# Optimization experiments

Measured on AMD Instinct MI355X. Metric: run time of the kernel, lower is better.

## Reference

```python
import jax, jax.numpy as jnp
import numpy as np

D_MODEL = 256
D_FFN = 1024
N_HEADS = 8
N_LEVELS = 4
N_POINTS = 4
SPATIAL = np.array([[60, 100], [30, 50], [15, 25], [8, 13]], dtype=np.int32)  # (H, W) per level


def _layer_norm(x, g, b, eps=1e-5):
    mu = jnp.mean(x, axis=-1, keepdims=True)
    var = jnp.mean(jnp.square(x - mu), axis=-1, keepdims=True)
    return (x - mu) * jax.lax.rsqrt(var + eps) * g + b


def _bilinear_sample(v_l, loc, aw, H, W):
    # v_l: (B,H,W,h,hd); loc: (B,Lq,h,p,2) normalized [0,1]; aw: (B,Lq,h,p)
    B = v_l.shape[0]
    h = v_l.shape[3]
    x = loc[..., 0] * W - 0.5  # grid_sample align_corners=False convention
    y = loc[..., 1] * H - 0.5
    x0 = jnp.floor(x)
    y0 = jnp.floor(y)
    lx = x - x0
    ly = y - y0
    x0i = x0.astype(jnp.int32)
    y0i = y0.astype(jnp.int32)
    bi = jnp.arange(B)[:, None, None, None]
    hi = jnp.arange(h)[None, None, :, None]

    def g(xi, yi):
        valid = (xi >= 0) & (xi < W) & (yi >= 0) & (yi < H)
        xc = jnp.clip(xi, 0, W - 1)
        yc = jnp.clip(yi, 0, H - 1)
        return v_l[bi, yc, xc, hi] * valid[..., None].astype(v_l.dtype)  # zero padding

    w00 = (1 - lx) * (1 - ly)
    w01 = lx * (1 - ly)
    w10 = (1 - lx) * ly
    w11 = lx * ly
    samp = (g(x0i, y0i) * w00[..., None] + g(x0i + 1, y0i) * w01[..., None]
            + g(x0i, y0i + 1) * w10[..., None] + g(x0i + 1, y0i + 1) * w11[..., None])
    # weighted sum over sampling points -> (B,Lq,h,hd)
    return jnp.einsum('blhpd,blhp->blhd', samp, aw)


def _msda(q, val, ref, W_value, b_value, W_off, b_off, W_attn, b_attn, W_out, b_out):
    # mmcv MultiScaleDeformableAttention (batch_first, identity=query, eval-mode dropout)
    B, Lq, C = q.shape
    hd = C // N_HEADS
    v = (val @ W_value + b_value).reshape(B, -1, N_HEADS, hd)
    off = (q @ W_off + b_off).reshape(B, Lq, N_HEADS, N_LEVELS, N_POINTS, 2)
    aw = jax.nn.softmax((q @ W_attn + b_attn).reshape(B, Lq, N_HEADS, N_LEVELS * N_POINTS), axis=-1)
    aw = aw.reshape(B, Lq, N_HEADS, N_LEVELS, N_POINTS)
    normalizer = jnp.asarray(SPATIAL[:, ::-1].copy(), dtype=q.dtype)  # (levels, 2) = (W, H)
    loc = ref[:, :, None, :, None, :] + off / normalizer[None, None, None, :, None, :]
    out = jnp.zeros((B, Lq, N_HEADS, hd), q.dtype)
    start = 0
    for lvl in range(N_LEVELS):
        H, W = int(SPATIAL[lvl, 0]), int(SPATIAL[lvl, 1])
        v_l = v[:, start:start + H * W].reshape(B, H, W, N_HEADS, hd)
        start += H * W
        out = out + _bilinear_sample(v_l, loc[:, :, :, lvl], aw[:, :, :, lvl], H, W)
    return q + out.reshape(B, Lq, C) @ W_out + b_out  # identity + output_proj


def setup_inputs() -> dict:
    key = jax.random.key(0)
    ks = jax.random.split(key, 16)
    bs, cams, nq = 1, 6, 6400
    l = int(SPATIAL.prod(axis=1).sum())
    s = 0.02
    inp = {
        'query': jax.random.normal(ks[0], (bs, nq, D_MODEL), jnp.float32),
        'key': jax.random.normal(ks[1], (bs, cams, l, D_MODEL), jnp.float32),
        'value': jax.random.normal(ks[2], (bs, cams, l, D_MODEL), jnp.float32),
        'reference_points_cam': jax.random.uniform(ks[3], (cams, bs, nq, N_LEVELS, 2), jnp.float32),
        'spatial_shapes': jnp.asarray(SPATIAL),
        'level_start_index': jnp.asarray(np.concatenate([[0], np.cumsum(SPATIAL.prod(axis=1))[:-1]]).astype(np.int32)),
        'bev_mask': jax.random.randint(ks[4], (cams, bs, nq, 4), 0, 2).astype(jnp.int32),
        'W_value': jax.random.normal(ks[5], (D_MODEL, D_MODEL), jnp.float32) * s,
        'b_value': jnp.zeros((D_MODEL,), jnp.float32),
        'W_off': jax.random.normal(ks[6], (D_MODEL, N_HEADS * N_LEVELS * N_POINTS * 2), jnp.float32) * s,
        'b_off': jax.random.normal(ks[7], (N_HEADS * N_LEVELS * N_POINTS * 2,), jnp.float32) * s,
        'W_attn': jax.random.normal(ks[8], (D_MODEL, N_HEADS * N_LEVELS * N_POINTS), jnp.float32) * s,
        'b_attn': jnp.zeros((N_HEADS * N_LEVELS * N_POINTS,), jnp.float32),
        'W_out': jax.random.normal(ks[9], (D_MODEL, D_MODEL), jnp.float32) * s,
        'b_out': jnp.zeros((D_MODEL,), jnp.float32),
        'ln1_g': jnp.ones((D_MODEL,), jnp.float32),
        'ln1_b': jnp.zeros((D_MODEL,), jnp.float32),
        'W1': jax.random.normal(ks[10], (D_MODEL, D_FFN), jnp.float32) * s,
        'b1': jnp.zeros((D_FFN,), jnp.float32),
        'W2': jax.random.normal(ks[11], (D_FFN, D_MODEL), jnp.float32) * s,
        'b2': jnp.zeros((D_MODEL,), jnp.float32),
        'ln2_g': jnp.ones((D_MODEL,), jnp.float32),
        'ln2_b': jnp.zeros((D_MODEL,), jnp.float32),
    }
    return inp


def reference(query, key, value, reference_points_cam, spatial_shapes, level_start_index, bev_mask,
              W_value, b_value, W_off, b_off, W_attn, b_attn, W_out, b_out,
              ln1_g, ln1_b, W1, b1, W2, b2, ln2_g, ln2_b):
    bs, nq, C = query.shape
    cams = key.shape[1]
    l = key.shape[2]
    # per-camera query visibility taken from batch element 0 (as in original)
    cam_mask = (bev_mask[:, 0].sum(-1) > 0).astype(query.dtype)  # (cams, nq)
    # rebatch via masking: equivalent to gather-to-padded since attention is per-query
    q_rb = (query[:, None] * cam_mask[None, :, :, None]).reshape(bs * cams, nq, C)
    ref_rb = (jnp.transpose(reference_points_cam, (1, 0, 2, 3, 4))
              * cam_mask[None, :, :, None, None]).reshape(bs * cams, nq, N_LEVELS, 2)
    val = value.reshape(bs * cams, l, C)
    attn = _msda(q_rb, val, ref_rb, W_value, b_value, W_off, b_off, W_attn, b_attn, W_out, b_out)
    attn = attn.reshape(bs, cams, nq, C)
    # scatter-add back (only visible camera contributions)
    slots = jnp.einsum('bknc,kn->bnc', attn, cam_mask)
    # visibility count (full bev_mask, per batch element)
    count = (bev_mask.sum(-1) > 0).astype(query.dtype)  # (cams, bs, nq)
    count = jnp.maximum(count.transpose(1, 2, 0).sum(-1), 1.0)  # (bs, nq)
    slots = slots / count[..., None]
    x = _layer_norm(slots + query, ln1_g, ln1_b)
    ffn = jax.nn.relu(x @ W1 + b1) @ W2 + b2
    return _layer_norm(x + ffn, ln2_g, ln2_b)
```

## Files before the change

kernel.cpp:

```cpp
#include <hip/hip_runtime.h>
#include <math.h>

#define NQ      6400
#define NCAMS   6
#define LTOT    7979
#define DM      256
#define DFFN    1024

typedef __attribute__((ext_vector_type(8))) short bf16x8;
typedef __attribute__((ext_vector_type(4))) float f32x4;

__device__ inline unsigned short f32_to_bf16(float f) {
    unsigned u = __float_as_uint(f);
    unsigned r = u + 0x7FFF + ((u >> 16) & 1);
    return (unsigned short)(r >> 16);
}

__global__ __launch_bounds__(256) void wt_kernel(
    const float* __restrict__ Wv, const float* __restrict__ Woff,
    const float* __restrict__ Wattn, const float* __restrict__ Wout,
    const float* __restrict__ W1, const float* __restrict__ W2,
    unsigned short* __restrict__ wsT)
{
    int b = blockIdx.x;
    const float* src; int K, N, t0, dstoff;
    if (b < 64)       { src = Wv;    K = 256;  N = 256;  t0 = 0;   dstoff = 0; }
    else if (b < 128) { src = Woff;  K = 256;  N = 256;  t0 = 64;  dstoff = 65536; }
    else if (b < 160) { src = Wattn; K = 256;  N = 128;  t0 = 128; dstoff = 131072; }
    else if (b < 224) { src = Wout;  K = 256;  N = 256;  t0 = 160; dstoff = 163840; }
    else if (b < 480) { src = W1;    K = 256;  N = 1024; t0 = 224; dstoff = 229376; }
    else              { src = W2;    K = 1024; N = 256;  t0 = 480; dstoff = 491520; }
    int t = b - t0;
    int ntn = N >> 5;
    int kt = t / ntn, nt = t - kt * ntn;
    __shared__ float tile[32][33];
    int tx = threadIdx.x & 31, ty = threadIdx.x >> 5;
    #pragma unroll
    for (int i = 0; i < 4; ++i)
        tile[ty + i * 8][tx] = src[(size_t)(kt * 32 + ty + i * 8) * N + nt * 32 + tx];
    __syncthreads();
    #pragma unroll
    for (int i = 0; i < 4; ++i) {
        int nn = nt * 32 + ty + i * 8;
        wsT[dstoff + (size_t)nn * K + kt * 32 + tx] = f32_to_bf16(tile[tx][ty + i * 8]);
    }
}

__global__ __launch_bounds__(256) void gemm_v_kernel(
    const float* __restrict__ A, const unsigned short* __restrict__ BT,
    const float* __restrict__ bias, unsigned short* __restrict__ Cb, int M)
{
    const int K = 256;
    __shared__ __align__(16) unsigned short As[128][40];
    __shared__ __align__(16) unsigned short Bs[128][40];

    const int tid  = threadIdx.x;
    const int wave = tid >> 6, lane = tid & 63;
    const int wm = wave >> 1, wn = wave & 1;
    const int quad = lane >> 4, l16 = lane & 15;
    const int m0 = blockIdx.y * 128, n0 = blockIdx.x * 128;

    f32x4 acc[4][4] = {};

    for (int k0 = 0; k0 < K; k0 += 32) {
        #pragma unroll
        for (int i = 0; i < 2; ++i) {
            int idx = tid + 256 * i;
            int r = idx >> 2, kc = (idx & 3) * 8;
            int gr = m0 + r;
            float4 f0, f1;
            if (gr < M) {
                f0 = *(const float4*)(A + (size_t)gr * K + k0 + kc);
                f1 = *(const float4*)(A + (size_t)gr * K + k0 + kc + 4);
            } else { f0 = make_float4(0,0,0,0); f1 = f0; }
            uint4 o;
            o.x = f32_to_bf16(f0.x) | ((unsigned)f32_to_bf16(f0.y) << 16);
            o.y = f32_to_bf16(f0.z) | ((unsigned)f32_to_bf16(f0.w) << 16);
            o.z = f32_to_bf16(f1.x) | ((unsigned)f32_to_bf16(f1.y) << 16);
            o.w = f32_to_bf16(f1.z) | ((unsigned)f32_to_bf16(f1.w) << 16);
            *(uint4*)&As[r][kc] = o;
        }
        #pragma unroll
        for (int i = 0; i < 2; ++i) {
            int idx = tid + 256 * i;
            int r = idx >> 2, kc = (idx & 3) * 8;
            *(uint4*)&Bs[r][kc] = *(const uint4*)(BT + (size_t)(n0 + r) * K + k0 + kc);
        }
        __syncthreads();
        bf16x8 af[4], bfr[4];
        #pragma unroll
        for (int mi = 0; mi < 4; ++mi)
            af[mi] = *(const bf16x8*)&As[wm * 64 + mi * 16 + l16][quad * 8];
        #pragma unroll
        for (int ni = 0; ni < 4; ++ni)
            bfr[ni] = *(const bf16x8*)&Bs[wn * 64 + ni * 16 + l16][quad * 8];
        #pragma unroll
        for (int mi = 0; mi < 4; ++mi)
            #pragma unroll
            for (int ni = 0; ni < 4; ++ni)
                acc[mi][ni] = __builtin_amdgcn_mfma_f32_16x16x32_bf16(
                    af[mi], bfr[ni], acc[mi][ni], 0, 0, 0);
        __syncthreads();
    }

    #pragma unroll
    for (int mi = 0; mi < 4; ++mi) {
        #pragma unroll
        for (int r = 0; r < 4; ++r) {
            int gm = m0 + wm * 64 + mi * 16 + quad * 4 + r;
            if (gm >= M) continue;
            int cam = gm / LTOT;
            int pix = gm - cam * LTOT;
            #pragma unroll
            for (int ni = 0; ni < 4; ++ni) {
                int gn = n0 + wn * 64 + ni * 16 + l16;
                int head = gn >> 5, ch = gn & 31;
                float v = acc[mi][ni][r] + bias[gn];
                Cb[(((size_t)(cam * 8 + head)) * LTOT + pix) * 32 + ch] = f32_to_bf16(v);
            }
        }
    }
}

__global__ __launch_bounds__(256) void qproj_kernel(
    const float* __restrict__ A, const unsigned short* __restrict__ WqT,
    const float* __restrict__ b_off, const float* __restrict__ b_attn,
    float* __restrict__ qoff, float* __restrict__ qaw)
{
    const int K = 256;
    __shared__ __align__(16) unsigned short As[64][40];
    __shared__ __align__(16) unsigned short Bs[128][40];

    const int tid  = threadIdx.x;
    const int wave = tid >> 6, lane = tid & 63;
    const int wm = wave >> 1, wn = wave & 1;
    const int quad = lane >> 4, l16 = lane & 15;
    const int m0 = blockIdx.y * 64, n0 = blockIdx.x * 128;
    const int is_attn = (n0 == 256);

    f32x4 acc[2][4] = {};

    for (int k0 = 0; k0 < K; k0 += 32) {
        {
            int r = tid >> 2, kc = (tid & 3) * 8;
            float4 f0 = *(const float4*)(A + (size_t)(m0 + r) * K + k0 + kc);
            float4 f1 = *(const float4*)(A + (size_t)(m0 + r) * K + k0 + kc + 4);
            uint4 o;
            o.x = f32_to_bf16(f0.x) | ((unsigned)f32_to_bf16(f0.y) << 16);
            o.y = f32_to_bf16(f0.z) | ((unsigned)f32_to_bf16(f0.w) << 16);
            o.z = f32_to_bf16(f1.x) | ((unsigned)f32_to_bf16(f1.y) << 16);
            o.w = f32_to_bf16(f1.z) | ((unsigned)f32_to_bf16(f1.w) << 16);
            *(uint4*)&As[r][kc] = o;
        }
        #pragma unroll
        for (int i = 0; i < 2; ++i) {
            int idx = tid + 256 * i;
            int r = idx >> 2, kc = (idx & 3) * 8;
            *(uint4*)&Bs[r][kc] = *(const uint4*)(WqT + (size_t)(n0 + r) * K + k0 + kc);
        }
        __syncthreads();
        bf16x8 af[2], bfr[4];
        #pragma unroll
        for (int mi = 0; mi < 2; ++mi)
            af[mi] = *(const bf16x8*)&As[wm * 32 + mi * 16 + l16][quad * 8];
        #pragma unroll
        for (int ni = 0; ni < 4; ++ni)
            bfr[ni] = *(const bf16x8*)&Bs[wn * 64 + ni * 16 + l16][quad * 8];
        #pragma unroll
        for (int mi = 0; mi < 2; ++mi)
            #pragma unroll
            for (int ni = 0; ni < 4; ++ni)
                acc[mi][ni] = __builtin_amdgcn_mfma_f32_16x16x32_bf16(
                    af[mi], bfr[ni], acc[mi][ni], 0, 0, 0);
        __syncthreads();
    }

    if (is_attn) {
        #pragma unroll
        for (int mi = 0; mi < 2; ++mi) {
            #pragma unroll
            for (int r = 0; r < 4; ++r) {
                int gm = m0 + wm * 32 + mi * 16 + quad * 4 + r;
                #pragma unroll
                for (int ni = 0; ni < 4; ++ni) {
                    int gn = wn * 64 + ni * 16 + l16;
                    float v = acc[mi][ni][r] + b_attn[gn];
                    float mx = v;
                    #pragma unroll
                    for (int s = 1; s < 16; s <<= 1)
                        mx = fmaxf(mx, __shfl_xor(mx, s, 64));
                    float e = __expf(v - mx);
                    float sum = e;
                    #pragma unroll
                    for (int s = 1; s < 16; s <<= 1)
                        sum += __shfl_xor(sum, s, 64);
                    qaw[(size_t)gm * 128 + gn] = e / sum;
                }
            }
        }
    } else {
        #pragma unroll
        for (int mi = 0; mi < 2; ++mi) {
            #pragma unroll
            for (int r = 0; r < 4; ++r) {
                int gm = m0 + wm * 32 + mi * 16 + quad * 4 + r;
                #pragma unroll
                for (int ni = 0; ni < 4; ++ni) {
                    int gn = n0 + wn * 64 + ni * 16 + l16;
                    qoff[(size_t)gm * 256 + gn] = acc[mi][ni][r] + b_off[gn];
                }
            }
        }
    }
}

__global__ __launch_bounds__(256) void sample_kernel(
    const unsigned short* __restrict__ vb,
    const float* __restrict__ qoff,
    const float* __restrict__ aw,
    const float* __restrict__ refpts,
    const int*   __restrict__ bev_mask,
    unsigned short* __restrict__ outsum,
    float* __restrict__ visb)
{
    const int bid = blockIdx.x;
    const int h   = bid & 7;
    const int q0  = (bid >> 3) * 16;
    const int tid = threadIdx.x;
    const int sq  = tid >> 4;
    const int tup = tid & 15;
    const int lvl = tup >> 2;
    const int n_s = q0 + sq;
    const int tg  = (tid >> 2) & 3;
    const int cg  = tid & 3;

    __shared__ int2  s_tab[2][4][272];
    __shared__ float s_vis[NCAMS][16];
    __shared__ int   s_cnt[NCAMS];
    __shared__ int   s_nvis[16];

    if (tid < 96) {
        int cam = tid >> 4, q = tid & 15;
        const int* bm = bev_mask + ((size_t)cam * NQ + q0 + q) * 4;
        s_vis[cam][q] = ((bm[0] + bm[1] + bm[2] + bm[3]) > 0) ? 1.f : 0.f;
    }
    __syncthreads();
    if (tid < NCAMS) {
        float s = 0.f;
        #pragma unroll
        for (int q = 0; q < 16; ++q) s += s_vis[tid][q];
        s_cnt[tid] = (int)s;
    }
    if (tid >= 32 && tid < 48) {
        int q = tid - 32;
        float s = 0.f;
        #pragma unroll
        for (int cam = 0; cam < NCAMS; ++cam) s += s_vis[cam][q];
        s_nvis[q] = (int)s;
    }
    __syncthreads();

    const float my_aw = aw[(size_t)n_s * 128 + h * 16 + tup];
    const float offx  = qoff[(size_t)n_s * 256 + h * 32 + tup * 2];
    const float offy  = qoff[(size_t)n_s * 256 + h * 32 + tup * 2 + 1];
    const int Wl   = (lvl == 0) ? 100 : (lvl == 1) ? 50 : (lvl == 2) ? 25 : 13;
    const int Hl   = (lvl == 0) ? 60  : (lvl == 1) ? 30 : (lvl == 2) ? 15 : 8;
    const int base = (lvl == 0) ? 0   : (lvl == 1) ? 6000 : (lvl == 2) ? 7500 : 7875;
    const float dx = offx / (float)Wl;
    const float dy = offy / (float)Hl;
    const int tabi = sq * 17 + tup;

    int vcams[NCAMS], nvc = 0;
    #pragma unroll
    for (int k = 0; k < NCAMS; ++k)
        if (s_cnt[k] > 0) vcams[nvc++] = k;

    auto build_tab = [&](int k, int buf) {
        const size_t rbase = (((size_t)k * NQ + n_s) * 4 + lvl) * 2;
        float fx = (refpts[rbase + 0] + dx) * (float)Wl - 0.5f;
        float fy = (refpts[rbase + 1] + dy) * (float)Hl - 0.5f;
        float x0f = floorf(fx), y0f = floorf(fy);
        float lx = fx - x0f, ly = fy - y0f;
        int x0 = (int)x0f, y0 = (int)y0f;
        int x1 = x0 + 1, y1 = y0 + 1;
        float wb = my_aw * s_vis[k][sq];
        float w00 = (1.f - lx) * (1.f - ly) * wb;
        float w01 = lx * (1.f - ly) * wb;
        float w10 = (1.f - lx) * ly * wb;
        float w11 = lx * ly * wb;
        bool vx0 = (x0 >= 0) & (x0 < Wl), vx1 = (x1 >= 0) & (x1 < Wl);
        bool vy0 = (y0 >= 0) & (y0 < Hl), vy1 = (y1 >= 0) & (y1 < Hl);
        s_tab[buf][0][tabi] = make_int2((vx0 & vy0) ? (base + y0 * Wl + x0) * 64 : 0,
                                        __float_as_int((vx0 & vy0) ? w00 : 0.f));
        s_tab[buf][1][tabi] = make_int2((vx1 & vy0) ? (base + y0 * Wl + x1) * 64 : 0,
                                        __float_as_int((vx1 & vy0) ? w01 : 0.f));
        s_tab[buf][2][tabi] = make_int2((vx0 & vy1) ? (base + y1 * Wl + x0) * 64 : 0,
                                        __float_as_int((vx0 & vy1) ? w10 : 0.f));
        s_tab[buf][3][tabi] = make_int2((vx1 & vy1) ? (base + y1 * Wl + x1) * 64 : 0,
                                        __float_as_int((vx1 & vy1) ? w11 : 0.f));
    };

    float a0 = 0.f, a1 = 0.f, a2 = 0.f, a3 = 0.f;
    float a4 = 0.f, a5 = 0.f, a6 = 0.f, a7 = 0.f;

    if (nvc > 0) build_tab(vcams[0], 0);
    __syncthreads();

    int pb = 0;
    for (int i = 0; i < nvc; ++i) {
        int k = vcams[i];
        if (i + 1 < nvc) build_tab(vcams[i + 1], pb ^ 1);
        const char* vkh = (const char*)vb + (size_t)(k * 8 + h) * (LTOT * 64) + cg * 16;
        #pragma unroll
        for (int j = 0; j < 4; ++j) {
            int ti = sq * 17 + tg * 4 + j;
            #pragma unroll
            for (int corner = 0; corner < 4; ++corner) {
                int2 t = s_tab[pb][corner][ti];
                float w = __int_as_float(t.y);
                uint4 d = *(const uint4*)(vkh + t.x);
                a0 += w * __uint_as_float(d.x << 16);
                a1 += w * __uint_as_float(d.x & 0xFFFF0000u);
                a2 += w * __uint_as_float(d.y << 16);
                a3 += w * __uint_as_float(d.y & 0xFFFF0000u);
                a4 += w * __uint_as_float(d.z << 16);
                a5 += w * __uint_as_float(d.z & 0xFFFF0000u);
                a6 += w * __uint_as_float(d.w << 16);
                a7 += w * __uint_as_float(d.w & 0xFFFF0000u);
            }
        }
        __syncthreads();
        pb ^= 1;
    }

    a0 += __shfl_xor(a0, 4, 64); a0 += __shfl_xor(a0, 8, 64);
    a1 += __shfl_xor(a1, 4, 64); a1 += __shfl_xor(a1, 8, 64);
    a2 += __shfl_xor(a2, 4, 64); a2 += __shfl_xor(a2, 8, 64);
    a3 += __shfl_xor(a3, 4, 64); a3 += __shfl_xor(a3, 8, 64);
    a4 += __shfl_xor(a4, 4, 64); a4 += __shfl_xor(a4, 8, 64);
    a5 += __shfl_xor(a5, 4, 64); a5 += __shfl_xor(a5, 8, 64);
    a6 += __shfl_xor(a6, 4, 64); a6 += __shfl_xor(a6, 8, 64);
    a7 += __shfl_xor(a7, 4, 64); a7 += __shfl_xor(a7, 8, 64);

    if ((tid & 12) == 0) {
        int nv = s_nvis[sq];
        float sc = 1.f / (float)(nv > 0 ? nv : 1);
        uint4 o;
        o.x = f32_to_bf16(a0 * sc) | ((unsigned)f32_to_bf16(a1 * sc) << 16);
        o.y = f32_to_bf16(a2 * sc) | ((unsigned)f32_to_bf16(a3 * sc) << 16);
        o.z = f32_to_bf16(a4 * sc) | ((unsigned)f32_to_bf16(a5 * sc) << 16);
        o.w = f32_to_bf16(a6 * sc) | ((unsigned)f32_to_bf16(a7 * sc) << 16);
        *(uint4*)(outsum + (size_t)n_s * 256 + h * 32 + cg * 8) = o;
    }
    if (h == 0 && tid < 16) visb[q0 + tid] = (s_nvis[tid] > 0) ? 1.f : 0.f;
}

__global__ __launch_bounds__(256) void projln1_kernel(
    const unsigned short* __restrict__ A, const unsigned short* __restrict__ BT,
    const float* __restrict__ query, const float* __restrict__ visb,
    const float* __restrict__ b_out, const float* __restrict__ g,
    const float* __restrict__ b,
    float* __restrict__ xout, unsigned short* __restrict__ xbf)
{
    const int K = 256;
    __shared__ __align__(16) unsigned short As[32][40];
    __shared__ __align__(16) unsigned short Bs[256][40];
    __shared__ float sred[2][4][4][2];
    __shared__ float ssred[2][4][4][2];
    __shared__ float s_mu[32], s_rs[32];

    const int tid  = threadIdx.x;
    const int wave = tid >> 6, lane = tid & 63;
    const int wm = wave >> 1, wn = wave & 1;
    const int quad = lane >> 4, l16 = lane & 15;
    const int m0 = blockIdx.x * 32;

    f32x4 acc[8] = {};

    for (int k0 = 0; k0 < K; k0 += 32) {
        {
            int r = tid >> 3, kc = (tid & 7) * 4;
            *(uint2*)&As[r][kc] = *(const uint2*)(A + (size_t)(m0 + r) * K + k0 + kc);
        }
        {
            const unsigned short* src = BT + (size_t)tid * K + k0;
            uint4 d0 = *(const uint4*)(src);
            uint4 d1 = *(const uint4*)(src + 8);
            uint4 d2 = *(const uint4*)(src + 16);
            uint4 d3 = *(const uint4*)(src + 24);
            *(uint4*)&Bs[tid][0]  = d0;
            *(uint4*)&Bs[tid][8]  = d1;
            *(uint4*)&Bs[tid][16] = d2;
            *(uint4*)&Bs[tid][24] = d3;
        }
        __syncthreads();
        bf16x8 af = *(const bf16x8*)&As[wm * 16 + l16][quad * 8];
        #pragma unroll
        for (int ni = 0; ni < 8; ++ni) {
            bf16x8 bfr = *(const bf16x8*)&Bs[wn * 128 + ni * 16 + l16][quad * 8];
            acc[ni] = __builtin_amdgcn_mfma_f32_16x16x32_bf16(af, bfr, acc[ni], 0, 0, 0);
        }
        __syncthreads();
    }

    float vals[8][4];
    #pragma unroll
    for (int r = 0; r < 4; ++r) {
        int gm = m0 + wm * 16 + quad * 4 + r;
        float vs = visb[gm];
        float s = 0.f, ss = 0.f;
        #pragma unroll
        for (int ni = 0; ni < 8; ++ni) {
            int gn = wn * 128 + ni * 16 + l16;
            float v = acc[ni][r] + vs * b_out[gn]
                    + query[(size_t)gm * 256 + gn] * (1.f + vs);
            vals[ni][r] = v;
            s += v; ss += v * v;
        }
        #pragma unroll
        for (int m = 1; m < 16; m <<= 1) {
            s  += __shfl_xor(s,  m, 64);
            ss += __shfl_xor(ss, m, 64);
        }
        if (l16 == 0) {
            sred[wm][quad][r][wn]  = s;
            ssred[wm][quad][r][wn] = ss;
        }
    }
    __syncthreads();
    if (tid < 32) {
        int lwm = tid >> 4, lq = (tid >> 2) & 3, lr = tid & 3;
        float s  = sred[lwm][lq][lr][0]  + sred[lwm][lq][lr][1];
        float ss = ssred[lwm][lq][lr][0] + ssred[lwm][lq][lr][1];
        float mu = s * (1.f / 256.f);
        float var = ss * (1.f / 256.f) - mu * mu;
        s_mu[tid] = mu;
        s_rs[tid] = rsqrtf(var + 1e-5f);
    }
    __syncthreads();

    #pragma unroll
    for (int r = 0; r < 4; ++r) {
        int rowl = wm * 16 + quad * 4 + r;
        int gm = m0 + rowl;
        float mu = s_mu[rowl], rs = s_rs[rowl];
        #pragma unroll
        for (int ni = 0; ni < 8; ++ni) {
            int gn = wn * 128 + ni * 16 + l16;
            float res = (vals[ni][r] - mu) * rs * g[gn] + b[gn];
            xout[(size_t)gm * 256 + gn] = res;
            xbf[(size_t)gm * 256 + gn] = f32_to_bf16(res);
        }
    }
}

__global__ __launch_bounds__(256) void gemm64_kernel(
    const unsigned short* __restrict__ A, const unsigned short* __restrict__ BT,
    const float* __restrict__ bias, float* __restrict__ C,
    unsigned short* __restrict__ Cb,
    int M, int N, int K, int mode)
{
    __shared__ __align__(16) unsigned short As[64][40];
    __shared__ __align__(16) unsigned short Bs[128][40];

    const int tid  = threadIdx.x;
    const int wave = tid >> 6, lane = tid & 63;
    const int wm = wave >> 1, wn = wave & 1;
    const int quad = lane >> 4, l16 = lane & 15;
    const int m0 = blockIdx.y * 64, n0 = blockIdx.x * 128;
    const int nz = gridDim.z;
    const int klen = K / nz;
    const int kbase = blockIdx.z * klen;

    f32x4 acc[2][4] = {};

    for (int k0 = kbase; k0 < kbase + klen; k0 += 32) {
        {
            int r = tid >> 2, kc = (tid & 3) * 8;
            int gr = m0 + r;
            uint4 d = (gr < M) ? *(const uint4*)(A + (size_t)gr * K + k0 + kc)
                               : make_uint4(0u, 0u, 0u, 0u);
            *(uint4*)&As[r][kc] = d;
        }
        #pragma unroll
        for (int i = 0; i < 2; ++i) {
            int idx = tid + 256 * i;
            int r = idx >> 2, kc = (idx & 3) * 8;
            *(uint4*)&Bs[r][kc] = *(const uint4*)(BT + (size_t)(n0 + r) * K + k0 + kc);
        }
        __syncthreads();
        bf16x8 af[2], bfr[4];
        #pragma unroll
        for (int mi = 0; mi < 2; ++mi)
            af[mi] = *(const bf16x8*)&As[wm * 32 + mi * 16 + l16][quad * 8];
        #pragma unroll
        for (int ni = 0; ni < 4; ++ni)
            bfr[ni] = *(const bf16x8*)&Bs[wn * 64 + ni * 16 + l16][quad * 8];
        #pragma unroll
        for (int mi = 0; mi < 2; ++mi)
            #pragma unroll
            for (int ni = 0; ni < 4; ++ni)
                acc[mi][ni] = __builtin_amdgcn_mfma_f32_16x16x32_bf16(
                    af[mi], bfr[ni], acc[mi][ni], 0, 0, 0);
        __syncthreads();
    }

    const float* bz = (blockIdx.z == 0) ? bias : nullptr;
    float* Cz = C ? (C + (size_t)blockIdx.z * M * N) : nullptr;

    #pragma unroll
    for (int mi = 0; mi < 2; ++mi) {
        #pragma unroll
        for (int r = 0; r < 4; ++r) {
            int gm = m0 + wm * 32 + mi * 16 + quad * 4 + r;
            if (gm >= M) continue;
            #pragma unroll
            for (int ni = 0; ni < 4; ++ni) {
                int gn = n0 + wn * 64 + ni * 16 + l16;
                float v = acc[mi][ni][r] + (bz ? bz[gn] : 0.f);
                if (mode == 1) {
                    Cb[(size_t)gm * N + gn] = f32_to_bf16(fmaxf(v, 0.f));
                } else {
                    Cz[(size_t)gm * N + gn] = v;
                }
            }
        }
    }
}

__device__ inline float block_sum_256(float v, float* red)
{
    #pragma unroll
    for (int o = 32; o > 0; o >>= 1) v += __shfl_down(v, o, 64);
    int lane = threadIdx.x & 63, w = threadIdx.x >> 6;
    if (lane == 0) red[w] = v;
    __syncthreads();
    float t = red[0] + red[1] + red[2] + red[3];
    __syncthreads();
    return t;
}

__global__ __launch_bounds__(256) void ln2_kernel(
    const float* __restrict__ x, const float* __restrict__ f0,
    const float* __restrict__ f1,
    const float* __restrict__ g, const float* __restrict__ b,
    float* __restrict__ out)
{
    __shared__ float red[4];
    int n = blockIdx.x, j = threadIdx.x;
    size_t idx = (size_t)n * 256 + j;
    float t = x[idx] + f0[idx] + f1[idx];
    float mu = block_sum_256(t, red) * (1.f / 256.f);
    float d = t - mu;
    float var = block_sum_256(d * d, red) * (1.f / 256.f);
    out[idx] = d * rsqrtf(var + 1e-5f) * g[j] + b[j];
}

extern "C" void kernel_launch(void* const* d_in, const int* in_sizes, int n_in,
                              void* d_out, int out_size, void* d_ws, size_t ws_size,
                              hipStream_t stream)
{
    const float* query   = (const float*)d_in[0];
    const float* value   = (const float*)d_in[2];
    const float* refpts  = (const float*)d_in[3];
    const int*   bevmask = (const int*)d_in[6];
    const float* W_value = (const float*)d_in[7];
    const float* b_value = (const float*)d_in[8];
    const float* W_off   = (const float*)d_in[9];
    const float* b_off   = (const float*)d_in[10];
    const float* W_attn  = (const float*)d_in[11];
    const float* b_attn  = (const float*)d_in[12];
    const float* W_out   = (const float*)d_in[13];
    const float* b_out   = (const float*)d_in[14];
    const float* ln1_g   = (const float*)d_in[15];
    const float* ln1_b   = (const float*)d_in[16];
    const float* W1      = (const float*)d_in[17];
    const float* b1      = (const float*)d_in[18];
    const float* W2      = (const float*)d_in[19];
    const float* b2      = (const float*)d_in[20];
    const float* ln2_g   = (const float*)d_in[21];
    const float* ln2_b   = (const float*)d_in[22];
    float* out = (float*)d_out;

    char* ws = (char*)d_ws;
    unsigned short* vb     = (unsigned short*)(ws + 0);
    float*          xbuf   = (float*)(ws + 0);
    unsigned short* xbf    = (unsigned short*)(ws + 7000000);
    unsigned short* hbf    = (unsigned short*)(ws + 11000000);
    float*          qoff   = (float*)(ws + 25000000);
    float*          qaw    = (float*)(ws + 32000000);
    unsigned short* outsum = (unsigned short*)(ws + 35300000);
    float*          visb   = (float*)(ws + 38600000);
    unsigned short* wsT    = (unsigned short*)(ws + 38700000);
    float*          ffnout = (float*)(ws + 41000000);

    unsigned short* WvT = wsT;
    unsigned short* WqT = wsT + 65536;
    unsigned short* WoT = wsT + 163840;
    unsigned short* W1T = wsT + 229376;
    unsigned short* W2T = wsT + 491520;

    const int MV = NCAMS * LTOT;

    wt_kernel<<<dim3(736), 256, 0, stream>>>(
        W_value, W_off, W_attn, W_out, W1, W2, wsT);
    gemm_v_kernel<<<dim3(2, (MV + 127) / 128), 256, 0, stream>>>(
        value, WvT, b_value, vb, MV);
    qproj_kernel<<<dim3(3, 100), 256, 0, stream>>>(
        query, WqT, b_off, b_attn, qoff, qaw);
    sample_kernel<<<dim3(3200), 256, 0, stream>>>(
        vb, qoff, qaw, refpts, bevmask, outsum, visb);
    projln1_kernel<<<dim3(200), 256, 0, stream>>>(
        outsum, WoT, query, visb, b_out, ln1_g, ln1_b, xbuf, xbf);
    gemm64_kernel<<<dim3(8, 100, 1), 256, 0, stream>>>(
        xbf, W1T, b1, nullptr, hbf, NQ, DFFN, 256, 1);
    gemm64_kernel<<<dim3(2, 100, 2), 256, 0, stream>>>(
        hbf, W2T, b2, ffnout, nullptr, NQ, 256, DFFN, 0);
    ln2_kernel<<<dim3(NQ), 256, 0, stream>>>(
        xbuf, ffnout, ffnout + (size_t)NQ * 256, ln2_g, ln2_b, out);
}
```

Baseline: 321.7 us.

## Fuse FFN2 with LayerNorm2, enlarge FFN1 tiles, precompute all camera sample tables

Replaces the split-K FFN2 GEMM and the separate LayerNorm kernel with one kernel. It computes a full 256-wide output row block, adds bias and residual, and applies LayerNorm in registers, which removes the fp32 partial-sum round trip and one launch. FFN1 now uses a specialised 128x128 tile kernel. The sampling kernel builds the tables for all six cameras up front instead of double-buffering, which removes per-camera barriers but enlarges shared memory use and does table work for cameras with no visible queries. The fused FFN2 grid has only 200 blocks with a long K loop, so parallelism may be low.

```diff
diff --git a/kernel.cpp b/kernel.cpp
--- a/kernel.cpp
+++ b/kernel.cpp
@@ -234,7 +234,7 @@
     const int tg  = (tid >> 2) & 3;
     const int cg  = tid & 3;
 
-    __shared__ int2  s_tab[2][4][272];
+    __shared__ int2  s_tab[NCAMS][4][272];
     __shared__ float s_vis[NCAMS][16];
     __shared__ int   s_cnt[NCAMS];
     __shared__ int   s_nvis[16];
@@ -258,7 +258,6 @@
         for (int cam = 0; cam < NCAMS; ++cam) s += s_vis[cam][q];
         s_nvis[q] = (int)s;
     }
-    __syncthreads();
 
     const float my_aw = aw[(size_t)n_s * 128 + h * 16 + tup];
     const float offx  = qoff[(size_t)n_s * 256 + h * 32 + tup * 2];
@@ -270,15 +269,16 @@
     const float dy = offy / (float)Hl;
     const int tabi = sq * 17 + tup;
 
-    int vcams[NCAMS], nvc = 0;
+    float2 rp[NCAMS];
     #pragma unroll
     for (int k = 0; k < NCAMS; ++k)
-        if (s_cnt[k] > 0) vcams[nvc++] = k;
-
-    auto build_tab = [&](int k, int buf) {
-        const size_t rbase = (((size_t)k * NQ + n_s) * 4 + lvl) * 2;
-        float fx = (refpts[rbase + 0] + dx) * (float)Wl - 0.5f;
-        float fy = (refpts[rbase + 1] + dy) * (float)Hl - 0.5f;
+        rp[k] = *(const float2*)(refpts + (((size_t)k * NQ + n_s) * 4 + lvl) * 2);
+    __syncthreads();
+
+    #pragma unroll
+    for (int k = 0; k < NCAMS; ++k) {
+        float fx = (rp[k].x + dx) * (float)Wl - 0.5f;
+        float fy = (rp[k].y + dy) * (float)Hl - 0.5f;
         float x0f = floorf(fx), y0f = floorf(fy);
         float lx = fx - x0f, ly = fy - y0f;
         int x0 = (int)x0f, y0 = (int)y0f;
@@ -290,33 +290,29 @@
         float w11 = lx * ly * wb;
         bool vx0 = (x0 >= 0) & (x0 < Wl), vx1 = (x1 >= 0) & (x1 < Wl);
         bool vy0 = (y0 >= 0) & (y0 < Hl), vy1 = (y1 >= 0) & (y1 < Hl);
-        s_tab[buf][0][tabi] = make_int2((vx0 & vy0) ? (base + y0 * Wl + x0) * 64 : 0,
-                                        __float_as_int((vx0 & vy0) ? w00 : 0.f));
-        s_tab[buf][1][tabi] = make_int2((vx1 & vy0) ? (base + y0 * Wl + x1) * 64 : 0,
-                                        __float_as_int((vx1 & vy0) ? w01 : 0.f));
-        s_tab[buf][2][tabi] = make_int2((vx0 & vy1) ? (base + y1 * Wl + x0) * 64 : 0,
-                                        __float_as_int((vx0 & vy1) ? w10 : 0.f));
-        s_tab[buf][3][tabi] = make_int2((vx1 & vy1) ? (base + y1 * Wl + x1) * 64 : 0,
-                                        __float_as_int((vx1 & vy1) ? w11 : 0.f));
-    };
+        s_tab[k][0][tabi] = make_int2((vx0 & vy0) ? (base + y0 * Wl + x0) * 64 : 0,
+                                      __float_as_int((vx0 & vy0) ? w00 : 0.f));
+        s_tab[k][1][tabi] = make_int2((vx1 & vy0) ? (base + y0 * Wl + x1) * 64 : 0,
+                                      __float_as_int((vx1 & vy0) ? w01 : 0.f));
+        s_tab[k][2][tabi] = make_int2((vx0 & vy1) ? (base + y1 * Wl + x0) * 64 : 0,
+                                      __float_as_int((vx0 & vy1) ? w10 : 0.f));
+        s_tab[k][3][tabi] = make_int2((vx1 & vy1) ? (base + y1 * Wl + x1) * 64 : 0,
+                                      __float_as_int((vx1 & vy1) ? w11 : 0.f));
+    }
+    __syncthreads();
 
     float a0 = 0.f, a1 = 0.f, a2 = 0.f, a3 = 0.f;
     float a4 = 0.f, a5 = 0.f, a6 = 0.f, a7 = 0.f;
 
-    if (nvc > 0) build_tab(vcams[0], 0);
-    __syncthreads();
-
-    int pb = 0;
-    for (int i = 0; i < nvc; ++i) {
-        int k = vcams[i];
-        if (i + 1 < nvc) build_tab(vcams[i + 1], pb ^ 1);
+    for (int k = 0; k < NCAMS; ++k) {
+        if (s_cnt[k] == 0) continue;
         const char* vkh = (const char*)vb + (size_t)(k * 8 + h) * (LTOT * 64) + cg * 16;
         #pragma unroll
         for (int j = 0; j < 4; ++j) {
             int ti = sq * 17 + tg * 4 + j;
             #pragma unroll
             for (int corner = 0; corner < 4; ++corner) {
-                int2 t = s_tab[pb][corner][ti];
+                int2 t = s_tab[k][corner][ti];
                 float w = __int_as_float(t.y);
                 uint4 d = *(const uint4*)(vkh + t.x);
                 a0 += w * __uint_as_float(d.x << 16);
@@ -329,8 +325,6 @@
                 a7 += w * __uint_as_float(d.w & 0xFFFF0000u);
             }
         }
-        __syncthreads();
-        pb ^= 1;
     }
 
     a0 += __shfl_xor(a0, 4, 64); a0 += __shfl_xor(a0, 8, 64);
@@ -384,14 +378,10 @@
         }
         {
             const unsigned short* src = BT + (size_t)tid * K + k0;
-            uint4 d0 = *(const uint4*)(src);
-            uint4 d1 = *(const uint4*)(src + 8);
-            uint4 d2 = *(const uint4*)(src + 16);
-            uint4 d3 = *(const uint4*)(src + 24);
-            *(uint4*)&Bs[tid][0]  = d0;
-            *(uint4*)&Bs[tid][8]  = d1;
-            *(uint4*)&Bs[tid][16] = d2;
-            *(uint4*)&Bs[tid][24] = d3;
+            *(uint4*)&Bs[tid][0]  = *(const uint4*)(src);
+            *(uint4*)&Bs[tid][8]  = *(const uint4*)(src + 8);
+            *(uint4*)&Bs[tid][16] = *(const uint4*)(src + 16);
+            *(uint4*)&Bs[tid][24] = *(const uint4*)(src + 24);
         }
         __syncthreads();
         bf16x8 af = *(const bf16x8*)&As[wm * 16 + l16][quad * 8];
@@ -454,33 +444,28 @@
     }
 }
 
-__global__ __launch_bounds__(256) void gemm64_kernel(
+__global__ __launch_bounds__(256) void gemm_ffn1_kernel(
     const unsigned short* __restrict__ A, const unsigned short* __restrict__ BT,
-    const float* __restrict__ bias, float* __restrict__ C,
-    unsigned short* __restrict__ Cb,
-    int M, int N, int K, int mode)
-{
-    __shared__ __align__(16) unsigned short As[64][40];
+    const float* __restrict__ bias, unsigned short* __restrict__ Cb)
+{
+    const int K = 256, N = DFFN;
+    __shared__ __align__(16) unsigned short As[128][40];
     __shared__ __align__(16) unsigned short Bs[128][40];
 
     const int tid  = threadIdx.x;
     const int wave = tid >> 6, lane = tid & 63;
     const int wm = wave >> 1, wn = wave & 1;
     const int quad = lane >> 4, l16 = lane & 15;
-    const int m0 = blockIdx.y * 64, n0 = blockIdx.x * 128;
-    const int nz = gridDim.z;
-    const int klen = K / nz;
-    const int kbase = blockIdx.z * klen;
-
-    f32x4 acc[2][4] = {};
-
-    for (int k0 = kbase; k0 < kbase + klen; k0 += 32) {
-        {
-            int r = tid >> 2, kc = (tid & 3) * 8;
-            int gr = m0 + r;
-            uint4 d = (gr < M) ? *(const uint4*)(A + (size_t)gr * K + k0 + kc)
-                               : make_uint4(0u, 0u, 0u, 0u);
-            *(uint4*)&As[r][kc] = d;
+    const int m0 = blockIdx.y * 128, n0 = blockIdx.x * 128;
+
+    f32x4 acc[4][4] = {};
+
+    for (int k0 = 0; k0 < K; k0 += 32) {
+        #pragma unroll
+        for (int i = 0; i < 2; ++i) {
+            int idx = tid + 256 * i;
+            int r = idx >> 2, kc = (idx & 3) * 8;
+            *(uint4*)&As[r][kc] = *(const uint4*)(A + (size_t)(m0 + r) * K + k0 + kc);
         }
         #pragma unroll
         for (int i = 0; i < 2; ++i) {
@@ -489,15 +474,15 @@
             *(uint4*)&Bs[r][kc] = *(const uint4*)(BT + (size_t)(n0 + r) * K + k0 + kc);
         }
         __syncthreads();
-        bf16x8 af[2], bfr[4];
-        #pragma unroll
-        for (int mi = 0; mi < 2; ++mi)
-            af[mi] = *(const bf16x8*)&As[wm * 32 + mi * 16 + l16][quad * 8];
+        bf16x8 af[4], bfr[4];
+        #pragma unroll
+        for (int mi = 0; mi < 4; ++mi)
+            af[mi] = *(const bf16x8*)&As[wm * 64 + mi * 16 + l16][quad * 8];
         #pragma unroll
         for (int ni = 0; ni < 4; ++ni)
             bfr[ni] = *(const bf16x8*)&Bs[wn * 64 + ni * 16 + l16][quad * 8];
         #pragma unroll
-        for (int mi = 0; mi < 2; ++mi)
+        for (int mi = 0; mi < 4; ++mi)
             #pragma unroll
             for (int ni = 0; ni < 4; ++ni)
                 acc[mi][ni] = __builtin_amdgcn_mfma_f32_16x16x32_bf16(
@@ -505,55 +490,109 @@
         __syncthreads();
     }
 
-    const float* bz = (blockIdx.z == 0) ? bias : nullptr;
-    float* Cz = C ? (C + (size_t)blockIdx.z * M * N) : nullptr;
-
-    #pragma unroll
-    for (int mi = 0; mi < 2; ++mi) {
+    #pragma unroll
+    for (int mi = 0; mi < 4; ++mi) {
         #pragma unroll
         for (int r = 0; r < 4; ++r) {
-            int gm = m0 + wm * 32 + mi * 16 + quad * 4 + r;
-            if (gm >= M) continue;
+            int gm = m0 + wm * 64 + mi * 16 + quad * 4 + r;
             #pragma unroll
             for (int ni = 0; ni < 4; ++ni) {
                 int gn = n0 + wn * 64 + ni * 16 + l16;
-                float v = acc[mi][ni][r] + (bz ? bz[gn] : 0.f);
-                if (mode == 1) {
-                    Cb[(size_t)gm * N + gn] = f32_to_bf16(fmaxf(v, 0.f));
-                } else {
-                    Cz[(size_t)gm * N + gn] = v;
-                }
+                float v = acc[mi][ni][r] + bias[gn];
+                Cb[(size_t)gm * N + gn] = f32_to_bf16(fmaxf(v, 0.f));
             }
         }
     }
 }
 
-__device__ inline float block_sum_256(float v, float* red)
-{
-    #pragma unroll
-    for (int o = 32; o > 0; o >>= 1) v += __shfl_down(v, o, 64);
-    int lane = threadIdx.x & 63, w = threadIdx.x >> 6;
-    if (lane == 0) red[w] = v;
-    __syncthreads();
-    float t = red[0] + red[1] + red[2] + red[3];
-    __syncthreads();
-    return t;
-}
-
-__global__ __launch_bounds__(256) void ln2_kernel(
-    const float* __restrict__ x, const float* __restrict__ f0,
-    const float* __restrict__ f1,
+__global__ __launch_bounds__(256) void projln2_kernel(
+    const unsigned short* __restrict__ A, const unsigned short* __restrict__ BT,
+    const float* __restrict__ xres, const float* __restrict__ bias,
     const float* __restrict__ g, const float* __restrict__ b,
     float* __restrict__ out)
 {
-    __shared__ float red[4];
-    int n = blockIdx.x, j = threadIdx.x;
-    size_t idx = (size_t)n * 256 + j;
-    float t = x[idx] + f0[idx] + f1[idx];
-    float mu = block_sum_256(t, red) * (1.f / 256.f);
-    float d = t - mu;
-    float var = block_sum_256(d * d, red) * (1.f / 256.f);
-    out[idx] = d * rsqrtf(var + 1e-5f) * g[j] + b[j];
+    const int K = DFFN;
+    __shared__ __align__(16) unsigned short As[32][40];
+    __shared__ __align__(16) unsigned short Bs[256][40];
+    __shared__ float sred[2][4][4][2];
+    __shared__ float ssred[2][4][4][2];
+    __shared__ float s_mu[32], s_rs[32];
+
+    const int tid  = threadIdx.x;
+    const int wave = tid >> 6, lane = tid & 63;
+    const int wm = wave >> 1, wn = wave & 1;
+    const int quad = lane >> 4, l16 = lane & 15;
+    const int m0 = blockIdx.x * 32;
+
+    f32x4 acc[8] = {};
+
+    for (int k0 = 0; k0 < K; k0 += 32) {
+        {
+            int r = tid >> 3, kc = (tid & 7) * 4;
+            *(uint2*)&As[r][kc] = *(const uint2*)(A + (size_t)(m0 + r) * K + k0 + kc);
+        }
+        {
+            const unsigned short* src = BT + (size_t)tid * K + k0;
+            *(uint4*)&Bs[tid][0]  = *(const uint4*)(src);
+            *(uint4*)&Bs[tid][8]  = *(const uint4*)(src + 8);
+            *(uint4*)&Bs[tid][16] = *(const uint4*)(src + 16);
+            *(uint4*)&Bs[tid][24] = *(const uint4*)(src + 24);
+        }
+        __syncthreads();
+        bf16x8 af = *(const bf16x8*)&As[wm * 16 + l16][quad * 8];
+        #pragma unroll
+        for (int ni = 0; ni < 8; ++ni) {
+            bf16x8 bfr = *(const bf16x8*)&Bs[wn * 128 + ni * 16 + l16][quad * 8];
+            acc[ni] = __builtin_amdgcn_mfma_f32_16x16x32_bf16(af, bfr, acc[ni], 0, 0, 0);
+        }
+        __syncthreads();
+    }
+
+    float vals[8][4];
+    #pragma unroll
+    for (int r = 0; r < 4; ++r) {
+        int gm = m0 + wm * 16 + quad * 4 + r;
+        float s = 0.f, ss = 0.f;
+        #pragma unroll
+        for (int ni = 0; ni < 8; ++ni) {
+            int gn = wn * 128 + ni * 16 + l16;
+            float v = acc[ni][r] + bias[gn] + xres[(size_t)gm * 256 + gn];
+            vals[ni][r] = v;
+            s += v; ss += v * v;
+        }
+        #pragma unroll
+        for (int m = 1; m < 16; m <<= 1) {
+            s  += __shfl_xor(s,  m, 64);
+            ss += __shfl_xor(ss, m, 64);
+        }
+        if (l16 == 0) {
+            sred[wm][quad][r][wn]  = s;
+            ssred[wm][quad][r][wn] = ss;
+        }
+    }
+    __syncthreads();
+    if (tid < 32) {
+        int lwm = tid >> 4, lq = (tid >> 2) & 3, lr = tid & 3;
+        float s  = sred[lwm][lq][lr][0]  + sred[lwm][lq][lr][1];
+        float ss = ssred[lwm][lq][lr][0] + ssred[lwm][lq][lr][1];
+        float mu = s * (1.f / 256.f);
+        float var = ss * (1.f / 256.f) - mu * mu;
+        s_mu[tid] = mu;
+        s_rs[tid] = rsqrtf(var + 1e-5f);
+    }
+    __syncthreads();
+
+    #pragma unroll
+    for (int r = 0; r < 4; ++r) {
+        int rowl = wm * 16 + quad * 4 + r;
+        int gm = m0 + rowl;
+        float mu = s_mu[rowl], rs = s_rs[rowl];
+        #pragma unroll
+        for (int ni = 0; ni < 8; ++ni) {
+            int gn = wn * 128 + ni * 16 + l16;
+            out[(size_t)gm * 256 + gn] = (vals[ni][r] - mu) * rs * g[gn] + b[gn];
+        }
+    }
 }
 
 extern "C" void kernel_launch(void* const* d_in, const int* in_sizes, int n_in,
@@ -592,7 +631,6 @@
     unsigned short* outsum = (unsigned short*)(ws + 35300000);
     float*          visb   = (float*)(ws + 38600000);
     unsigned short* wsT    = (unsigned short*)(ws + 38700000);
-    float*          ffnout = (float*)(ws + 41000000);
 
     unsigned short* WvT = wsT;
     unsigned short* WqT = wsT + 65536;
@@ -612,10 +650,8 @@
         vb, qoff, qaw, refpts, bevmask, outsum, visb);
     projln1_kernel<<<dim3(200), 256, 0, stream>>>(
         outsum, WoT, query, visb, b_out, ln1_g, ln1_b, xbuf, xbf);
-    gemm64_kernel<<<dim3(8, 100, 1), 256, 0, stream>>>(
-        xbf, W1T, b1, nullptr, hbf, NQ, DFFN, 256, 1);
-    gemm64_kernel<<<dim3(2, 100, 2), 256, 0, stream>>>(
-        hbf, W2T, b2, ffnout, nullptr, NQ, 256, DFFN, 0);
-    ln2_kernel<<<dim3(NQ), 256, 0, stream>>>(
-        xbuf, ffnout, ffnout + (size_t)NQ * 256, ln2_g, ln2_b, out);
-}
+    gemm_ffn1_kernel<<<dim3(8, 50), 256, 0, stream>>>(
+        xbf, W1T, b1, hbf);
+    projln2_kernel<<<dim3(200), 256, 0, stream>>>(
+        hbf, W2T, xbuf, b2, ln2_g, ln2_b, out);
+}
```

After: 330.8 us. 2.8% more time.
